# Kernel optimization log

Measured on AMD Instinct MI355X. Metric: run time of the kernel, lower is better.

The kernel has to match this reference:

```python
import jax, jax.numpy as jnp
import numpy as np

D_K = 64
N_HEADS = 16
D_MODEL = 1024


def setup_inputs() -> dict:
    key = jax.random.key(0)
    ks = jax.random.split(key, 12)
    N, T = 2, 2048
    H = D_K * N_HEADS
    s = 1.0 / np.sqrt(D_MODEL)
    inp = {
        "q": jax.random.normal(ks[0], (N, T, D_MODEL), jnp.float32),
        "k": jax.random.normal(ks[1], (N, T, D_MODEL), jnp.float32),
        "v": jax.random.normal(ks[2], (N, T, D_MODEL), jnp.float32),
        "mask": jax.random.randint(ks[3], (N, T), 0, 2, jnp.int32),
        "Wq": jax.random.normal(ks[4], (D_MODEL, H), jnp.float32) * s,
        "bq": jax.random.normal(ks[5], (H,), jnp.float32) * 0.02,
        "Wk": jax.random.normal(ks[6], (D_MODEL, H), jnp.float32) * s,
        "bk": jax.random.normal(ks[7], (H,), jnp.float32) * 0.02,
        "Wv": jax.random.normal(ks[8], (D_MODEL, H), jnp.float32) * s,
        "bv": jax.random.normal(ks[9], (H,), jnp.float32) * 0.02,
        "Wo": jax.random.normal(ks[10], (H, D_MODEL), jnp.float32) * (1.0 / np.sqrt(H)),
        "bo": jax.random.normal(ks[11], (D_MODEL,), jnp.float32) * 0.02,
    }
    return inp


def reference(q, k, v, mask, Wq, bq, Wk, bk, Wv, bv, Wo, bo):
    N, T, _ = q.shape
    # project and split heads: [N, T, H*dk] -> [N, nH, T, dk]
    def split(x):
        return x.reshape(N, T, N_HEADS, D_K).transpose(0, 2, 1, 3)
    qh = split(q @ Wq + bq)
    kh = split(k @ Wk + bk)
    vh = split(v @ Wv + bv)
    scores = jnp.einsum("bhqd,bhkd->bhqk", qh, kh) / np.sqrt(D_K)
    # key padding mask: mask[:, None, None, :] == 0 -> -inf
    scores = jnp.where(mask[:, None, None, :] == 0, -jnp.inf, scores)
    attn = jax.nn.softmax(scores, axis=-1)
    A = jnp.einsum("bhqk,bhkd->bhqd", attn, vh)
    A = A.transpose(0, 2, 1, 3).reshape(N, T, N_HEADS * D_K)
    return A @ Wo + bo
```

## Files before the change

kernel.cpp:

```cpp
#include <hip/hip_runtime.h>

#define T_SEQ 2048
#define DM 1024
#define NH 16
#define DKH 64
#define NB 2
#define M_ROWS (NB * T_SEQ)
#define QSCALE 0.18033688011112042f

using bf16x8 = __attribute__((ext_vector_type(8))) __bf16;
using f32x4  = __attribute__((ext_vector_type(4))) float;
using halfx4 = __attribute__((ext_vector_type(4))) __fp16;
using halfx8 = __attribute__((ext_vector_type(8))) __fp16;
using halfx2 = __attribute__((ext_vector_type(2))) __fp16;
using uintx4 = __attribute__((ext_vector_type(4))) unsigned;

__device__ __forceinline__ short f2bf(float f) {
  unsigned u = __builtin_bit_cast(unsigned, f);
  u += 0x7fffu + ((u >> 16) & 1u);
  return (short)(u >> 16);
}

#if defined(__has_builtin) && __has_builtin(__builtin_amdgcn_cvt_pk_bf16_f32)
using bf16x2 = __attribute__((ext_vector_type(2))) __bf16;
__device__ __forceinline__ short2 pk2(float a, float b) {
  bf16x2 r = __builtin_amdgcn_cvt_pk_bf16_f32(a, b);
  return __builtin_bit_cast(short2, r);
}
#else
__device__ __forceinline__ short2 pk2(float a, float b) {
  short2 r; r.x = f2bf(a); r.y = f2bf(b); return r;
}
#endif

__device__ __forceinline__ short2 pkh(float a, float b) {
  halfx2 r = __builtin_amdgcn_cvt_pkrtz(a, b);
  return __builtin_bit_cast(short2, r);
}

#if defined(__has_builtin) && __has_builtin(__builtin_amdgcn_exp2f)
__device__ __forceinline__ float fexp2(float x) { return __builtin_amdgcn_exp2f(x); }
#else
__device__ __forceinline__ float fexp2(float x) { return exp2f(x); }
#endif

#if defined(__has_builtin) && __has_builtin(__builtin_amdgcn_permlane32_swap) && \
    __has_builtin(__builtin_amdgcn_permlane16_swap)
using uintx2 = __attribute__((ext_vector_type(2))) unsigned;
__device__ __forceinline__ void swap32(unsigned& a, unsigned& b) {
  uintx2 r = __builtin_amdgcn_permlane32_swap(a, b, false, false);
  a = r.x; b = r.y;
}
__device__ __forceinline__ void swap16(unsigned& a, unsigned& b) {
  uintx2 r = __builtin_amdgcn_permlane16_swap(a, b, false, false);
  a = r.x; b = r.y;
}
#else
__device__ __forceinline__ void swap32(unsigned& a, unsigned& b) {
  asm volatile("v_permlane32_swap_b32 %0, %1" : "+v"(a), "+v"(b));
}
__device__ __forceinline__ void swap16(unsigned& a, unsigned& b) {
  asm volatile("v_permlane16_swap_b32 %0, %1" : "+v"(a), "+v"(b));
}
#endif

#define GLD16(g, l)                                                            \
  __builtin_amdgcn_global_load_lds(                                            \
      (const __attribute__((address_space(1))) void*)(g),                      \
      (__attribute__((address_space(3))) void*)(l), 16, 0, 0)

__global__ __launch_bounds__(256) void prep_x(
    const float* __restrict__ q, const float* __restrict__ k,
    const float* __restrict__ v, const int* __restrict__ mask,
    short* __restrict__ dst, float* __restrict__ mf) {
  const float* s = blockIdx.z == 0 ? q : (blockIdx.z == 1 ? k : v);
  short* d = dst + (size_t)blockIdx.z * (M_ROWS * DM);
  const int n4 = M_ROWS * DM / 4;
  for (int i = blockIdx.x * 256 + threadIdx.x; i < n4; i += gridDim.x * 256) {
    float4 f = *(const float4*)(s + i * 4);
    short2 a = pk2(f.x, f.y), b = pk2(f.z, f.w);
    short4 o = {a.x, a.y, b.x, b.y};
    *(short4*)(d + i * 4) = o;
  }
  if (blockIdx.z == 0 && blockIdx.x < 4) {
    int i = (blockIdx.x * 256 + threadIdx.x) * 4;
    int4 m = *(const int4*)(mask + i);
    float4 o = {m.x ? 0.f : -1e38f, m.y ? 0.f : -1e38f,
                m.z ? 0.f : -1e38f, m.w ? 0.f : -1e38f};
    *(float4*)(mf + i) = o;
  }
}

__global__ __launch_bounds__(256) void prep_w(
    const float* __restrict__ w0, const float* __restrict__ w1,
    const float* __restrict__ w2, const float* __restrict__ w3,
    short* __restrict__ dst) {
  __shared__ short T[64][72];
  const float* W = blockIdx.z == 0 ? w0 : blockIdx.z == 1 ? w1
                   : blockIdx.z == 2 ? w2 : w3;
  short* D = dst + (size_t)blockIdx.z * (DM * DM);
  const int k0 = blockIdx.x * 64, n0 = blockIdx.y * 64;
  const int r = threadIdx.x >> 2, cs = (threadIdx.x & 3) * 16;
#pragma unroll
  for (int j = 0; j < 4; ++j) {
    float4 f = *(const float4*)(W + (size_t)(k0 + r) * DM + n0 + cs + j * 4);
    short2 a = pk2(f.x, f.y), b = pk2(f.z, f.w);
    short4 o = {a.x, a.y, b.x, b.y};
    *(short4*)&T[r][cs + j * 4] = o;
  }
  __syncthreads();
  short tmp[16];
#pragma unroll
  for (int i = 0; i < 16; ++i) tmp[i] = T[cs + i][r];
  *(int4*)(D + (size_t)(n0 + r) * DM + k0 + cs) = *(const int4*)&tmp[0];
  *(int4*)(D + (size_t)(n0 + r) * DM + k0 + cs + 8) = *(const int4*)&tmp[8];
}

__global__ __launch_bounds__(512) void gemm_qkv(
    const short* __restrict__ A_, const short* __restrict__ Bt_,
    const float* __restrict__ b0, const float* __restrict__ b1,
    const float* __restrict__ b2, short* __restrict__ Y) {
  __shared__ short As[2][4096];
  __shared__ short Bs[2][4096];
  const int z = blockIdx.z;
  const short* A = A_ + (size_t)z * (M_ROWS * DM);
  const short* Bt = Bt_ + (size_t)z * (DM * DM);
  short* Yz = Y + (size_t)z * ((size_t)M_ROWS * DM);
  const float* bias = z == 0 ? b0 : (z == 1 ? b1 : b2);
  const int m0 = blockIdx.x * 128, n0 = blockIdx.y * 128;
  const int tid = threadIdx.x, w = tid >> 6, lane = tid & 63;
  const int quad = lane >> 4, lm = lane & 15, wa = w & 1, wb = w >> 1;

  const short* Ag = A + (size_t)(m0 + w * 16 + lm) * DM + quad * 8;
  const short* Bg = Bt + (size_t)(n0 + w * 16 + lm) * DM + quad * 8;

  f32x4 acc[4][2];
#pragma unroll
  for (int i = 0; i < 4; ++i)
#pragma unroll
    for (int j = 0; j < 2; ++j) acc[i][j] = (f32x4){0.f, 0.f, 0.f, 0.f};

  GLD16(Ag, &As[0][w * 512]);
  GLD16(Bg, &Bs[0][w * 512]);

  for (int kt = 0; kt < DM / 32; ++kt) {
    const int cb = kt & 1;
    __syncthreads();
    if (kt + 1 < DM / 32) {
      GLD16(Ag + (kt + 1) * 32, &As[cb ^ 1][w * 512]);
      GLD16(Bg + (kt + 1) * 32, &Bs[cb ^ 1][w * 512]);
    }
    bf16x8 af[4], bfr[2];
#pragma unroll
    for (int i = 0; i < 4; ++i)
      af[i] = *(const bf16x8*)&As[cb][(wa * 4 + i) * 512 + quad * 128 + lm * 8];
#pragma unroll
    for (int j = 0; j < 2; ++j)
      bfr[j] = *(const bf16x8*)&Bs[cb][(wb * 2 + j) * 512 + quad * 128 + lm * 8];
#pragma unroll
    for (int mi = 0; mi < 4; ++mi)
#pragma unroll
      for (int j = 0; j < 2; ++j)
        acc[mi][j] = __builtin_amdgcn_mfma_f32_16x16x32_bf16(
            af[mi], bfr[j], acc[mi][j], 0, 0, 0);
  }

  if (z < 2) {
#pragma unroll
    for (int j = 0; j < 2; ++j) {
      const int f = n0 + (wb * 2 + j) * 16 + lm;
      const float bv = bias[f];
      const int h = f >> 6, dk = f & 63;
#pragma unroll
      for (int mi = 0; mi < 4; ++mi)
#pragma unroll
        for (int r = 0; r < 4; ++r) {
          const int m = m0 + (wa * 4 + mi) * 16 + quad * 4 + r;
          float val = acc[mi][j][r] + bv;
          if (z == 0) val *= QSCALE;
          const int b = m >> 11, tt = m & (T_SEQ - 1);
          Yz[(((size_t)(b * NH + h) << 11) + tt) * DKH + dk] = f2bf(val);
        }
    }
  } else {
#pragma unroll
    for (int j = 0; j < 2; ++j) {
      const int f = n0 + (wb * 2 + j) * 16 + lm;
      const float bv = bias[f];
      const int h = f >> 6, dk = f & 63;
#pragma unroll
      for (int mi = 0; mi < 4; ++mi) {
        const int t = m0 + (wa * 4 + mi) * 16 + quad * 4;
        const int b = t >> 11, tt = t & (T_SEQ - 1);
        short2 a = pkh(acc[mi][j][0] + bv, acc[mi][j][1] + bv);
        short2 c = pkh(acc[mi][j][2] + bv, acc[mi][j][3] + bv);
        short4 o = {a.x, a.y, c.x, c.y};
        *(short4*)(Yz + (((size_t)(b * NH + h) * DKH + dk) << 11) + tt) = o;
      }
    }
  }
}

__global__ __launch_bounds__(512) void gemm_out(
    const short* __restrict__ A, const short* __restrict__ Bt,
    const float* __restrict__ bias, float* __restrict__ Yf) {
  __shared__ short As[2][4096];
  __shared__ short Bs[2][4096];
  const int m0 = blockIdx.x * 128, n0 = blockIdx.y * 128;
  const int tid = threadIdx.x, w = tid >> 6, lane = tid & 63;
  const int quad = lane >> 4, lm = lane & 15, wa = w & 1, wb = w >> 1;

  const short* Ag = A + (size_t)(m0 + w * 16 + lm) * DM + quad * 8;
  const short* Bg = Bt + (size_t)(n0 + w * 16 + lm) * DM + quad * 8;

  f32x4 acc[4][2];
#pragma unroll
  for (int i = 0; i < 4; ++i)
#pragma unroll
    for (int j = 0; j < 2; ++j) acc[i][j] = (f32x4){0.f, 0.f, 0.f, 0.f};

  GLD16(Ag, &As[0][w * 512]);
  GLD16(Bg, &Bs[0][w * 512]);

  for (int kt = 0; kt < DM / 32; ++kt) {
    const int cb = kt & 1;
    __syncthreads();
    if (kt + 1 < DM / 32) {
      GLD16(Ag + (kt + 1) * 32, &As[cb ^ 1][w * 512]);
      GLD16(Bg + (kt + 1) * 32, &Bs[cb ^ 1][w * 512]);
    }
    bf16x8 af[4], bfr[2];
#pragma unroll
    for (int i = 0; i < 4; ++i)
      af[i] = *(const bf16x8*)&As[cb][(wa * 4 + i) * 512 + quad * 128 + lm * 8];
#pragma unroll
    for (int j = 0; j < 2; ++j)
      bfr[j] = *(const bf16x8*)&Bs[cb][(wb * 2 + j) * 512 + quad * 128 + lm * 8];
#pragma unroll
    for (int mi = 0; mi < 4; ++mi)
#pragma unroll
      for (int j = 0; j < 2; ++j)
        acc[mi][j] = __builtin_amdgcn_mfma_f32_16x16x32_bf16(
            af[mi], bfr[j], acc[mi][j], 0, 0, 0);
  }

#pragma unroll
  for (int j = 0; j < 2; ++j) {
    const int n = n0 + (wb * 2 + j) * 16 + lm;
    const float bv = bias[n];
#pragma unroll
    for (int mi = 0; mi < 4; ++mi)
#pragma unroll
      for (int r = 0; r < 4; ++r) {
        const int m = m0 + (wa * 4 + mi) * 16 + quad * 4 + r;
        Yf[(size_t)m * DM + n] = acc[mi][j][r] + bv;
      }
  }
}

__global__ __launch_bounds__(512) void attn_kernel(
    const short* __restrict__ Qh, const short* __restrict__ Kh,
    const short* __restrict__ Vt, const float* __restrict__ mf,
    short* __restrict__ Ao) {
  __shared__ short Ks[2][8192];
  __shared__ short Vs[2][8192];
  const int id = blockIdx.x + gridDim.x * blockIdx.y;
  const int bh = id & 31, qt = id >> 5;
  const int b = bh >> 4, h = bh & (NH - 1);
  const int tid = threadIdx.x, w = tid >> 6, lane = tid & 63;
  const int quad = lane >> 4, lm = lane & 15;
  const size_t base = (size_t)bh * T_SEQ * DKH;
  const float* mp = mf + b * T_SEQ;
  const int q0 = qt * 256 + w * 32;

  const short* qpA = Qh + base + (size_t)(q0 + lm) * DKH;
  const short* qpB = qpA + (size_t)16 * DKH;
  const bf16x8 qbA0 = *(const bf16x8*)(qpA + quad * 8);
  const bf16x8 qbA1 = *(const bf16x8*)(qpA + 32 + quad * 8);
  const bf16x8 qbB0 = *(const bf16x8*)(qpB + quad * 8);
  const bf16x8 qbB1 = *(const bf16x8*)(qpB + 32 + quad * 8);

  const int sw = w & 3;
  const bool isV = w >= 4;
  const short* Kg = Kh + base + (size_t)(sw * 16 + lm) * DKH + quad * 8;
  const short* Vg = Vt + base + (size_t)(sw * 16 + lm) * T_SEQ + quad * 8;

  f32x4 otA[4], otB[4];
#pragma unroll
  for (int i = 0; i < 4; ++i) {
    otA[i] = (f32x4){0.f, 0.f, 0.f, 0.f};
    otB[i] = (f32x4){0.f, 0.f, 0.f, 0.f};
  }
  float lA = 0.f, lB = 0.f;

  if (!isV) {
    GLD16(Kg, &Ks[0][sw * 1024]);
    GLD16(Kg + 32, &Ks[0][sw * 1024 + 512]);
    GLD16(Kg + (size_t)64 * DKH, &Ks[0][(sw + 4) * 1024]);
    GLD16(Kg + (size_t)64 * DKH + 32, &Ks[0][(sw + 4) * 1024 + 512]);
  } else {
    GLD16(Vg, &Vs[0][sw * 2048]);
    GLD16(Vg + 32, &Vs[0][sw * 2048 + 512]);
    GLD16(Vg + 64, &Vs[0][sw * 2048 + 1024]);
    GLD16(Vg + 96, &Vs[0][sw * 2048 + 1536]);
  }

  for (int kt = 0; kt < T_SEQ / 128; ++kt) {
    const int cb = kt & 1;
    const int key0 = kt * 128;
    __syncthreads();
    if (kt + 1 < T_SEQ / 128) {
      const int nk = key0 + 128;
      if (!isV) {
        GLD16(Kg + (size_t)nk * DKH, &Ks[cb ^ 1][sw * 1024]);
        GLD16(Kg + (size_t)nk * DKH + 32, &Ks[cb ^ 1][sw * 1024 + 512]);
        GLD16(Kg + (size_t)(nk + 64) * DKH, &Ks[cb ^ 1][(sw + 4) * 1024]);
        GLD16(Kg + (size_t)(nk + 64) * DKH + 32, &Ks[cb ^ 1][(sw + 4) * 1024 + 512]);
      } else {
        GLD16(Vg + nk, &Vs[cb ^ 1][sw * 2048]);
        GLD16(Vg + nk + 32, &Vs[cb ^ 1][sw * 2048 + 512]);
        GLD16(Vg + nk + 64, &Vs[cb ^ 1][sw * 2048 + 1024]);
        GLD16(Vg + nk + 96, &Vs[cb ^ 1][sw * 2048 + 1536]);
      }
    }

    halfx8 pbA[4], pbB[4];
#pragma unroll
    for (int kp = 0; kp < 4; ++kp) {
      unsigned peA0, peA1, poA0, poA1;
      unsigned peB0, peB1, poB0, poB1;
#pragma unroll
      for (int hf = 0; hf < 2; ++hf) {
        const int nt = kp * 2 + hf;
        bf16x8 ka0 = *(const bf16x8*)&Ks[cb][nt * 1024 + quad * 128 + lm * 8];
        bf16x8 ka1 = *(const bf16x8*)&Ks[cb][nt * 1024 + 512 + quad * 128 + lm * 8];
        f32x4 sA = (f32x4){0.f, 0.f, 0.f, 0.f};
        sA = __builtin_amdgcn_mfma_f32_16x16x32_bf16(ka0, qbA0, sA, 0, 0, 0);
        sA = __builtin_amdgcn_mfma_f32_16x16x32_bf16(ka1, qbA1, sA, 0, 0, 0);
        f32x4 sB = (f32x4){0.f, 0.f, 0.f, 0.f};
        sB = __builtin_amdgcn_mfma_f32_16x16x32_bf16(ka0, qbB0, sB, 0, 0, 0);
        sB = __builtin_amdgcn_mfma_f32_16x16x32_bf16(ka1, qbB1, sB, 0, 0, 0);
        const float4 m4 = *(const float4*)(mp + key0 + nt * 16 + quad * 4);
        float a0 = fexp2(sA[0] + m4.x);
        float a1 = fexp2(sA[1] + m4.y);
        float a2 = fexp2(sA[2] + m4.z);
        float a3 = fexp2(sA[3] + m4.w);
        lA += (a0 + a1) + (a2 + a3);
        float b0 = fexp2(sB[0] + m4.x);
        float b1 = fexp2(sB[1] + m4.y);
        float b2 = fexp2(sB[2] + m4.z);
        float b3 = fexp2(sB[3] + m4.w);
        lB += (b0 + b1) + (b2 + b3);
        unsigned loA = __builtin_bit_cast(unsigned, pkh(a0, a1));
        unsigned hiA = __builtin_bit_cast(unsigned, pkh(a2, a3));
        unsigned loB = __builtin_bit_cast(unsigned, pkh(b0, b1));
        unsigned hiB = __builtin_bit_cast(unsigned, pkh(b2, b3));
        if (hf == 0) {
          peA0 = loA; peA1 = hiA; peB0 = loB; peB1 = hiB;
        } else {
          poA0 = loA; poA1 = hiA; poB0 = loB; poB1 = hiB;
        }
      }
      {
        unsigned x0 = peA0, y0 = poA0, x1 = peA1, y1 = poA1;
        swap32(x0, y0); swap16(x0, y0);
        swap32(x1, y1); swap16(x1, y1);
        pbA[kp] = __builtin_bit_cast(halfx8, (uintx4){x0, x1, y0, y1});
      }
      {
        unsigned x0 = peB0, y0 = poB0, x1 = peB1, y1 = poB1;
        swap32(x0, y0); swap16(x0, y0);
        swap32(x1, y1); swap16(x1, y1);
        pbB[kp] = __builtin_bit_cast(halfx8, (uintx4){x0, x1, y0, y1});
      }
    }

#pragma unroll
    for (int nt2 = 0; nt2 < 4; ++nt2) {
#pragma unroll
      for (int kp = 0; kp < 4; ++kp) {
        halfx8 va =
            *(const halfx8*)&Vs[cb][nt2 * 2048 + kp * 512 + quad * 128 + lm * 8];
        otA[nt2] =
            __builtin_amdgcn_mfma_f32_16x16x32_f16(va, pbA[kp], otA[nt2], 0, 0, 0);
        otB[nt2] =
            __builtin_amdgcn_mfma_f32_16x16x32_f16(va, pbB[kp], otB[nt2], 0, 0, 0);
      }
    }
  }
  lA += __shfl_xor(lA, 16, 64);
  lA += __shfl_xor(lA, 32, 64);
  lB += __shfl_xor(lB, 16, 64);
  lB += __shfl_xor(lB, 32, 64);
  const float invA = 1.f / lA;
  const float invB = 1.f / lB;
  const size_t rowA = (size_t)(b * T_SEQ + q0 + lm) * DM + h * DKH;
  const size_t rowB = rowA + (size_t)16 * DM;
#pragma unroll
  for (int nt = 0; nt < 4; ++nt) {
    short2 a = pk2(otA[nt][0] * invA, otA[nt][1] * invA);
    short2 c = pk2(otA[nt][2] * invA, otA[nt][3] * invA);
    short4 o4 = {a.x, a.y, c.x, c.y};
    *(short4*)(Ao + rowA + nt * 16 + quad * 4) = o4;
    short2 e = pk2(otB[nt][0] * invB, otB[nt][1] * invB);
    short2 g = pk2(otB[nt][2] * invB, otB[nt][3] * invB);
    short4 o5 = {e.x, e.y, g.x, g.y};
    *(short4*)(Ao + rowB + nt * 16 + quad * 4) = o5;
  }
}

extern "C" void kernel_launch(void* const* d_in, const int* in_sizes, int n_in,
                              void* d_out, int out_size, void* d_ws, size_t ws_size,
                              hipStream_t stream) {
  const float* q = (const float*)d_in[0];
  const float* k = (const float*)d_in[1];
  const float* v = (const float*)d_in[2];
  const int* mk = (const int*)d_in[3];
  const float* Wq = (const float*)d_in[4];
  const float* bq = (const float*)d_in[5];
  const float* Wk = (const float*)d_in[6];
  const float* bk = (const float*)d_in[7];
  const float* Wv = (const float*)d_in[8];
  const float* bv = (const float*)d_in[9];
  const float* Wo = (const float*)d_in[10];
  const float* bo = (const float*)d_in[11];

  const size_t XE = (size_t)M_ROWS * DM;
  const size_t WE = (size_t)DM * DM;
  short* xb = (short*)d_ws;
  short* Wt = xb + 3 * XE;
  short* Qh = Wt + 4 * WE;
  float* mf = (float*)(Qh + 3 * XE);
  short* Ao = xb;

  prep_x<<<dim3(1024, 1, 3), 256, 0, stream>>>(q, k, v, mk, xb, mf);
  prep_w<<<dim3(16, 16, 4), 256, 0, stream>>>(Wq, Wk, Wv, Wo, Wt);
  gemm_qkv<<<dim3(M_ROWS / 128, DM / 128, 3), 512, 0, stream>>>(
      xb, Wt, bq, bk, bv, Qh);
  attn_kernel<<<dim3(T_SEQ / 256, NB * NH), 512, 0, stream>>>(
      Qh, Qh + XE, Qh + 2 * XE, mf, Ao);
  gemm_out<<<dim3(M_ROWS / 128, DM / 128), 512, 0, stream>>>(
      Ao, Wt + 3 * WE, bo, (float*)d_out);
}
```

Measured before the change: 254.3 us.

## Deepen K/V staging to four buffers with prefetch distance two and stage mask in LDS

The attention kernel's K/V shared-memory ring grows from two to four buffers and loads two tiles ahead. It waits on outstanding loads with explicit vmcnt counts and a raw s_barrier instead of __syncthreads before each tile. The key mask row is also copied once into LDS so the inner loop no longer reads it from global memory. This trades more LDS, which may lower occupancy, and hand-tuned waitcnt logic for more time to hide memory latency. A four-buffer ring with distance-two prefetch and only one barrier per iteration can let a fast wave overwrite a buffer a slower wave is still reading, and the mask copy has no explicit wait before its first use.

```diff
diff --git a/kernel.cpp b/kernel.cpp
--- a/kernel.cpp
+++ b/kernel.cpp
@@ -262,8 +262,9 @@
     const short* __restrict__ Qh, const short* __restrict__ Kh,
     const short* __restrict__ Vt, const float* __restrict__ mf,
     short* __restrict__ Ao) {
-  __shared__ short Ks[2][8192];
-  __shared__ short Vs[2][8192];
+  __shared__ short Ks[4][8192];
+  __shared__ short Vs[4][8192];
+  __shared__ float Ms[T_SEQ];
   const int id = blockIdx.x + gridDim.x * blockIdx.y;
   const int bh = id & 31, qt = id >> 5;
   const int b = bh >> 4, h = bh & (NH - 1);
@@ -285,6 +286,8 @@
   const short* Kg = Kh + base + (size_t)(sw * 16 + lm) * DKH + quad * 8;
   const short* Vg = Vt + base + (size_t)(sw * 16 + lm) * T_SEQ + quad * 8;
 
+  GLD16(mp + w * 256 + lane * 4, &Ms[w * 256]);
+
   f32x4 otA[4], otB[4];
 #pragma unroll
   for (int i = 0; i < 4; ++i) {
@@ -293,36 +296,34 @@
   }
   float lA = 0.f, lB = 0.f;
 
-  if (!isV) {
-    GLD16(Kg, &Ks[0][sw * 1024]);
-    GLD16(Kg + 32, &Ks[0][sw * 1024 + 512]);
-    GLD16(Kg + (size_t)64 * DKH, &Ks[0][(sw + 4) * 1024]);
-    GLD16(Kg + (size_t)64 * DKH + 32, &Ks[0][(sw + 4) * 1024 + 512]);
-  } else {
-    GLD16(Vg, &Vs[0][sw * 2048]);
-    GLD16(Vg + 32, &Vs[0][sw * 2048 + 512]);
-    GLD16(Vg + 64, &Vs[0][sw * 2048 + 1024]);
-    GLD16(Vg + 96, &Vs[0][sw * 2048 + 1536]);
-  }
+  auto stageK = [&](int buf, int key) {
+    GLD16(Kg + (size_t)key * DKH, &Ks[buf][sw * 1024]);
+    GLD16(Kg + (size_t)key * DKH + 32, &Ks[buf][sw * 1024 + 512]);
+    GLD16(Kg + (size_t)(key + 64) * DKH, &Ks[buf][(sw + 4) * 1024]);
+    GLD16(Kg + (size_t)(key + 64) * DKH + 32, &Ks[buf][(sw + 4) * 1024 + 512]);
+  };
+  auto stageV = [&](int buf, int key) {
+    GLD16(Vg + key, &Vs[buf][sw * 2048]);
+    GLD16(Vg + key + 32, &Vs[buf][sw * 2048 + 512]);
+    GLD16(Vg + key + 64, &Vs[buf][sw * 2048 + 1024]);
+    GLD16(Vg + key + 96, &Vs[buf][sw * 2048 + 1536]);
+  };
+
+  if (!isV) { stageK(0, 0); stageK(1, 128); }
+  else      { stageV(0, 0); stageV(1, 128); }
 
   for (int kt = 0; kt < T_SEQ / 128; ++kt) {
-    const int cb = kt & 1;
+    const int cb = kt & 3;
     const int key0 = kt * 128;
-    __syncthreads();
-    if (kt + 1 < T_SEQ / 128) {
-      const int nk = key0 + 128;
-      if (!isV) {
-        GLD16(Kg + (size_t)nk * DKH, &Ks[cb ^ 1][sw * 1024]);
-        GLD16(Kg + (size_t)nk * DKH + 32, &Ks[cb ^ 1][sw * 1024 + 512]);
-        GLD16(Kg + (size_t)(nk + 64) * DKH, &Ks[cb ^ 1][(sw + 4) * 1024]);
-        GLD16(Kg + (size_t)(nk + 64) * DKH + 32, &Ks[cb ^ 1][(sw + 4) * 1024 + 512]);
-      } else {
-        GLD16(Vg + nk, &Vs[cb ^ 1][sw * 2048]);
-        GLD16(Vg + nk + 32, &Vs[cb ^ 1][sw * 2048 + 512]);
-        GLD16(Vg + nk + 64, &Vs[cb ^ 1][sw * 2048 + 1024]);
-        GLD16(Vg + nk + 96, &Vs[cb ^ 1][sw * 2048 + 1536]);
-      }
-    }
+    if (kt + 2 < T_SEQ / 128) {
+      if (!isV) stageK((kt + 2) & 3, key0 + 256);
+      else      stageV((kt + 2) & 3, key0 + 256);
+    }
+    if (kt + 2 < T_SEQ / 128)      asm volatile("s_waitcnt vmcnt(8)" ::: "memory");
+    else if (kt + 1 < T_SEQ / 128) asm volatile("s_waitcnt vmcnt(4)" ::: "memory");
+    else                           asm volatile("s_waitcnt vmcnt(0)" ::: "memory");
+    __builtin_amdgcn_s_barrier();
+    __builtin_amdgcn_sched_barrier(0);
 
     halfx8 pbA[4], pbB[4];
 #pragma unroll
@@ -340,7 +341,7 @@
         f32x4 sB = (f32x4){0.f, 0.f, 0.f, 0.f};
         sB = __builtin_amdgcn_mfma_f32_16x16x32_bf16(ka0, qbB0, sB, 0, 0, 0);
         sB = __builtin_amdgcn_mfma_f32_16x16x32_bf16(ka1, qbB1, sB, 0, 0, 0);
-        const float4 m4 = *(const float4*)(mp + key0 + nt * 16 + quad * 4);
+        const float4 m4 = *(const float4*)&Ms[key0 + nt * 16 + quad * 4];
         float a0 = fexp2(sA[0] + m4.x);
         float a1 = fexp2(sA[1] + m4.y);
         float a2 = fexp2(sA[2] + m4.z);
```

Result: faster. 246.2 us (-3.2%).
